# Performance work log

Measured on AMD Instinct MI355X. Metric: run time of the kernel, lower is better.

## Reference

```python
import jax, jax.numpy as jnp
import numpy as np

DIM = 1024

def setup_inputs() -> dict:
    key = jax.random.key(0)
    ks = jax.random.split(key, 7)
    s = 1.0 / np.sqrt(DIM)  # roughly match nn.Linear init scale
    return {
        "x": jax.random.normal(ks[0], (4, 2048, DIM), dtype=jnp.float32),
        "Wq": jax.random.normal(ks[1], (DIM, DIM), dtype=jnp.float32) * s,
        "bq": jax.random.normal(ks[2], (DIM,), dtype=jnp.float32) * s,
        "Wk": jax.random.normal(ks[3], (DIM, DIM), dtype=jnp.float32) * s,
        "bk": jax.random.normal(ks[4], (DIM,), dtype=jnp.float32) * s,
        "Wv": jax.random.normal(ks[5], (DIM, DIM), dtype=jnp.float32) * s,
        "bv": jax.random.normal(ks[6], (DIM,), dtype=jnp.float32) * s,
    }

def reference(x, Wq, bq, Wk, bk, Wv, bv):
    # torch Linear: y = x @ W.T + b
    C = x.shape[-1]
    scale = C ** (-0.5)
    q = jnp.einsum('bnc,dc->bnd', x, Wq) + bq
    k = jnp.einsum('bnc,dc->bnd', x, Wk) + bk
    v = jnp.einsum('bnc,dc->bnd', x, Wv) + bv
    attn = jnp.einsum('bnd,bmd->bnm', q, k) * scale  # [B,N,N]
    attn = jax.nn.softmax(attn, axis=-1)
    out = jnp.einsum('bnm,bmd->bnd', attn, v)
    return out
```

## Files before the change

### kernel.cpp

```cpp
#include <hip/hip_runtime.h>

#define SEQ  2048
#define DIM  1024
#define NTOK 8192
#define NQKV 3072

typedef __attribute__((ext_vector_type(8))) __bf16 bf16x8;
typedef __attribute__((ext_vector_type(4))) float  f32x4;

__device__ __forceinline__ unsigned short f2bf(float f) {
    unsigned int u = __float_as_uint(f);
    u += 0x7fffu + ((u >> 16) & 1u);
    return (unsigned short)(u >> 16);
}

__device__ __forceinline__ float bfu2f(unsigned int lo16) {
    return __uint_as_float(lo16 << 16);
}

__device__ __forceinline__ void load_lds_128(const unsigned short* g, unsigned short* l) {
    __builtin_amdgcn_global_load_lds(
        (const __attribute__((address_space(1))) void*)g,
        (__attribute__((address_space(3))) void*)l, 16, 0, 0);
}

#define BAR() asm volatile("s_barrier" ::: "memory")

template <int MODE>
__global__ __launch_bounds__(512, 2)
void gemm256(const unsigned short* __restrict__ A, const unsigned short* __restrict__ B,
             void* __restrict__ Cv,
             const float* __restrict__ b0v, const float* __restrict__ b1v,
             const float* __restrict__ b2v, unsigned short* __restrict__ vt,
             float* __restrict__ rsv,
             int K, int lda, int ldb, int ldc,
             long sA, long sB, long sC, float alpha)
{
    constexpr int AT = 256 * 64;
    constexpr int BT = 128 * 64;
    __shared__ __align__(16) unsigned short As[3 * AT];
    __shared__ __align__(16) unsigned short Bs[3 * BT];

    const int tid  = threadIdx.x;
    const int wave = tid >> 6;
    const int lane = tid & 63;
    const int l4   = lane & 15;
    const int lh   = lane >> 4;
    const int wm   = wave >> 1;
    const int wn   = wave & 1;

    const int m0 = blockIdx.x * 256;
    const int n0 = blockIdx.y * 128;
    const int z  = blockIdx.z;
    A += (long)z * sA;
    B += (long)z * sB;

    const int r0 = tid >> 3;
    const int gc = (tid & 7) ^ (r0 & 7);
    const unsigned short* Ag = A + (long)(m0 + r0) * lda + gc * 8;
    const unsigned short* Bg = B + (long)(n0 + r0) * ldb + gc * 8;
    unsigned short* Al = As + tid * 8;
    unsigned short* Bl = Bs + tid * 8;

    const int NT = K >> 6;

    auto stage = [&](int t, int slot, int ph) {
        const long kof = (long)t * 64;
        unsigned short* al = Al + slot * AT;
        unsigned short* bl = Bl + slot * BT;
        if (ph == 0) {
            load_lds_128(Ag + kof,                          al);
            load_lds_128(Ag + kof + (long)64 * lda,         al + 4096);
            load_lds_128(Bg + kof,                          bl);
        } else {
            load_lds_128(Ag + kof + (long)128 * lda,        al + 8192);
            load_lds_128(Ag + kof + (long)192 * lda,        al + 12288);
            load_lds_128(Bg + kof + (long)64 * ldb,         bl + 4096);
        }
    };

    const int aoff = (wm * 64 + l4) * 64;
    const int boff = (wn * 64 + l4) * 64;
    const int cs0  = ((0 + lh) ^ (lane & 7)) * 8;
    const int cs1  = ((4 + lh) ^ (lane & 7)) * 8;

    f32x4 acc[4][4] = {};
    bf16x8 a0[4], b0[4], a1[4], b1[4];

    auto ldfrag = [&](bf16x8 (&a)[4], bf16x8 (&b)[4],
                      const unsigned short* Ab, const unsigned short* Bb, int cs) {
#pragma unroll
        for (int mf = 0; mf < 4; ++mf) a[mf] = *(const bf16x8*)(Ab + mf * 1024 + cs);
#pragma unroll
        for (int nf = 0; nf < 4; ++nf) b[nf] = *(const bf16x8*)(Bb + nf * 1024 + cs);
    };
    auto mfma16 = [&](bf16x8 (&a)[4], bf16x8 (&b)[4]) {
        __builtin_amdgcn_s_setprio(1);
#pragma unroll
        for (int mf = 0; mf < 4; ++mf)
#pragma unroll
            for (int nf = 0; nf < 4; ++nf)
                acc[mf][nf] = __builtin_amdgcn_mfma_f32_16x16x32_bf16(
                    a[mf], b[nf], acc[mf][nf], 0, 0, 0);
        __builtin_amdgcn_s_setprio(0);
    };

    stage(0, 0, 0); stage(0, 0, 1);
    stage(1, 1, 0); stage(1, 1, 1);
    asm volatile("s_waitcnt vmcnt(6)" ::: "memory");
    BAR();
    ldfrag(a0, b0, As + aoff, Bs + boff, cs0);

    int sl = 0;
    for (int t = 0; t < NT; ++t) {
        const unsigned short* Ab = As + sl * AT + aoff;
        const unsigned short* Bb = Bs + sl * BT + boff;
        const int st  = (sl >= 1) ? sl - 1 : 2;
        const int nsl = (sl == 2) ? 0 : sl + 1;

        ldfrag(a1, b1, Ab, Bb, cs1);
        if (t + 2 < NT) stage(t + 2, st, 0);
        mfma16(a0, b0);

        if (t + 2 < NT) stage(t + 2, st, 1);
        asm volatile("s_waitcnt lgkmcnt(0)" ::: "memory");
        if (t < NT - 2) asm volatile("s_waitcnt vmcnt(6)" ::: "memory");
        else            asm volatile("s_waitcnt vmcnt(0)" ::: "memory");
        BAR();
        if (t + 1 < NT)
            ldfrag(a0, b0, As + nsl * AT + aoff, Bs + nsl * BT + boff, cs0);
        mfma16(a1, b1);
        sl = nsl;
    }

    const int r0c = m0 + wm * 64 + lh * 4;
    const int c0c = n0 + wn * 64 + l4;

    if (MODE == 0) {
        if (n0 >= 2048) {
#pragma unroll
            for (int nf = 0; nf < 4; ++nf) {
                const int d = c0c + nf * 16 - 2048;
                const float bias = b2v[d];
#pragma unroll
                for (int mf = 0; mf < 4; ++mf) {
                    const int row = r0c + mf * 16;
                    const int bb = row >> 11;
                    const int mm = row & 2047;
                    ushort4 u;
                    u.x = f2bf(acc[mf][nf][0] + bias);
                    u.y = f2bf(acc[mf][nf][1] + bias);
                    u.z = f2bf(acc[mf][nf][2] + bias);
                    u.w = f2bf(acc[mf][nf][3] + bias);
                    *(ushort4*)(vt + ((long)bb * DIM + d) * SEQ + mm) = u;
                }
            }
        } else {
            unsigned short* C16 = (unsigned short*)Cv;
#pragma unroll
            for (int nf = 0; nf < 4; ++nf) {
                const int col = c0c + nf * 16;
                const float bias = (col >= 1024) ? b1v[col - 1024] : b0v[col];
#pragma unroll
                for (int mf = 0; mf < 4; ++mf)
#pragma unroll
                    for (int r = 0; r < 4; ++r)
                        C16[(long)(r0c + mf * 16 + r) * ldc + col] =
                            f2bf(acc[mf][nf][r] + bias);
            }
        }
    } else if (MODE == 1) {
        float* C = (float*)Cv + (long)z * sC;
        const float* rsp = rsv + (long)z * SEQ;
#pragma unroll
        for (int mf = 0; mf < 4; ++mf) {
            const int rowb = r0c + mf * 16;
            const float4 rs4 = *(const float4*)(rsp + rowb);
            const float i0 = 1.0f / rs4.x, i1 = 1.0f / rs4.y;
            const float i2 = 1.0f / rs4.z, i3 = 1.0f / rs4.w;
#pragma unroll
            for (int nf = 0; nf < 4; ++nf) {
                const int col = c0c + nf * 16;
                C[(long)(rowb + 0) * ldc + col] = acc[mf][nf][0] * i0;
                C[(long)(rowb + 1) * ldc + col] = acc[mf][nf][1] * i1;
                C[(long)(rowb + 2) * ldc + col] = acc[mf][nf][2] * i2;
                C[(long)(rowb + 3) * ldc + col] = acc[mf][nf][3] * i3;
            }
        }
    } else {
        unsigned short* C16 = (unsigned short*)Cv + (long)z * sC;
        float* rs = rsv + (long)z * SEQ;
#pragma unroll
        for (int mf = 0; mf < 4; ++mf)
#pragma unroll
            for (int r = 0; r < 4; ++r) {
                const int rowi = r0c + mf * 16 + r;
                float s = 0.f;
#pragma unroll
                for (int nf = 0; nf < 4; ++nf) {
                    const int col = c0c + nf * 16;
                    const unsigned short pu = f2bf(__expf(acc[mf][nf][r] * alpha));
                    C16[(long)rowi * ldc + col] = pu;
                    s += bfu2f(pu);
                }
                s += __shfl_xor(s, 1);
                s += __shfl_xor(s, 2);
                s += __shfl_xor(s, 4);
                s += __shfl_xor(s, 8);
                if (l4 == 0) atomicAdd(rs + rowi, s);
            }
    }
}

#define PREP_BLOCKS (8192 + 3072 + 32)

__global__ __launch_bounds__(256)
void prep(const float* __restrict__ x,
          const float* __restrict__ Wq, const float* __restrict__ Wk,
          const float* __restrict__ Wv,
          unsigned short* __restrict__ xb, unsigned short* __restrict__ Wb,
          float* __restrict__ rs)
{
    const int b = blockIdx.x;
    if (b < 8192) {
        const int i = b * 256 + threadIdx.x;
        float4 f = ((const float4*)x)[i];
        ushort4 u;
        u.x = f2bf(f.x); u.y = f2bf(f.y); u.z = f2bf(f.z); u.w = f2bf(f.w);
        ((ushort4*)xb)[i] = u;
    } else if (b < 8192 + 3072) {
        const int idx = (b - 8192) * 256 + threadIdx.x;
        const int sel = idx / (DIM * DIM / 4);
        const int j   = idx - sel * (DIM * DIM / 4);
        const float* src = (sel == 0) ? Wq : ((sel == 1) ? Wk : Wv);
        float4 f = ((const float4*)src)[j];
        ushort4 u;
        u.x = f2bf(f.x); u.y = f2bf(f.y); u.z = f2bf(f.z); u.w = f2bf(f.w);
        ((ushort4*)(Wb + (long)sel * DIM * DIM))[j] = u;
    } else {
        const int idx = (b - 8192 - 3072) * 256 + threadIdx.x;
        if (idx < NTOK) rs[idx] = 0.f;
    }
}

extern "C" void kernel_launch(void* const* d_in, const int* in_sizes, int n_in,
                              void* d_out, int out_size, void* d_ws, size_t ws_size,
                              hipStream_t stream)
{
    const float* x  = (const float*)d_in[0];
    const float* Wq = (const float*)d_in[1];
    const float* bq = (const float*)d_in[2];
    const float* Wk = (const float*)d_in[3];
    const float* bk = (const float*)d_in[4];
    const float* Wv = (const float*)d_in[5];
    const float* bv = (const float*)d_in[6];
    float* out = (float*)d_out;

    char* ws = (char*)d_ws;
    unsigned short* xb   = (unsigned short*)ws;
    unsigned short* Wb   = (unsigned short*)(ws + 16u * 1024 * 1024);
    unsigned short* qkv  = (unsigned short*)(ws + 64u * 1024 * 1024);
    unsigned short* vt   = (unsigned short*)(ws + 112u * 1024 * 1024);
    unsigned short* P    = (unsigned short*)(ws + 128u * 1024 * 1024);
    float*          rs   = (float*)(ws + 160u * 1024 * 1024);

    const float scale = 0.03125f;
    dim3 blk512(512);

    prep<<<PREP_BLOCKS, 256, 0, stream>>>(x, Wq, Wk, Wv, xb, Wb, rs);

    gemm256<0><<<dim3(NTOK / 256, NQKV / 128), blk512, 0, stream>>>(
        xb, Wb, qkv, bq, bk, bv, vt, nullptr,
        DIM, DIM, DIM, NQKV, 0, 0, 0, 1.0f);

    gemm256<2><<<dim3(SEQ / 256, SEQ / 128, 4), blk512, 0, stream>>>(
        qkv, qkv + 1024, P, nullptr, nullptr, nullptr, nullptr, rs,
        DIM, NQKV, NQKV, SEQ,
        (long)SEQ * NQKV, (long)SEQ * NQKV, (long)SEQ * SEQ, scale);

    gemm256<1><<<dim3(SEQ / 256, DIM / 128, 4), blk512, 0, stream>>>(
        P, vt, out, nullptr, nullptr, nullptr, nullptr, rs,
        SEQ, SEQ, SEQ, DIM,
        (long)SEQ * SEQ, (long)DIM * SEQ, (long)SEQ * DIM, 1.0f);
}
```

Before: 243.6 us.

## Add dedicated triple-buffered PV GEMM kernel with fragment double-buffering

Replaces the generic gemm256<1> for the P·V product with a specialized kernel. It uses a three-slot LDS ring for asynchronous global-to-LDS loads, split into two phases per tile, and double-buffered register fragments so MFMA work overlaps both the LDS reads and the global loads. MFMA sections run at raised wave priority via s_setprio. The cost is more LDS per block (about 144KB for three stages), which may limit occupancy, and hand-tuned waitcnt logic that must match the number of outstanding loads.

```diff
diff --git a/kernel.cpp b/kernel.cpp
--- a/kernel.cpp
+++ b/kernel.cpp
@@ -169,24 +169,6 @@
                             f2bf(acc[mf][nf][r] + bias);
             }
         }
-    } else if (MODE == 1) {
-        float* C = (float*)Cv + (long)z * sC;
-        const float* rsp = rsv + (long)z * SEQ;
-#pragma unroll
-        for (int mf = 0; mf < 4; ++mf) {
-            const int rowb = r0c + mf * 16;
-            const float4 rs4 = *(const float4*)(rsp + rowb);
-            const float i0 = 1.0f / rs4.x, i1 = 1.0f / rs4.y;
-            const float i2 = 1.0f / rs4.z, i3 = 1.0f / rs4.w;
-#pragma unroll
-            for (int nf = 0; nf < 4; ++nf) {
-                const int col = c0c + nf * 16;
-                C[(long)(rowb + 0) * ldc + col] = acc[mf][nf][0] * i0;
-                C[(long)(rowb + 1) * ldc + col] = acc[mf][nf][1] * i1;
-                C[(long)(rowb + 2) * ldc + col] = acc[mf][nf][2] * i2;
-                C[(long)(rowb + 3) * ldc + col] = acc[mf][nf][3] * i3;
-            }
-        }
     } else {
         unsigned short* C16 = (unsigned short*)Cv + (long)z * sC;
         float* rs = rsv + (long)z * SEQ;
@@ -209,6 +191,130 @@
                 s += __shfl_xor(s, 8);
                 if (l4 == 0) atomicAdd(rs + rowi, s);
             }
+    }
+}
+
+__global__ __launch_bounds__(512, 2)
+void gemm_pv(const unsigned short* __restrict__ A, const unsigned short* __restrict__ B,
+             float* __restrict__ C, const float* __restrict__ rsv,
+             int K, int lda, int ldb, int ldc,
+             long sA, long sB, long sC)
+{
+    constexpr int AT = 256 * 64;
+    constexpr int BT = 128 * 64;
+    __shared__ __align__(16) unsigned short As[3 * AT];
+    __shared__ __align__(16) unsigned short Bs[3 * BT];
+
+    const int tid  = threadIdx.x;
+    const int wave = tid >> 6;
+    const int lane = tid & 63;
+    const int l4   = lane & 15;
+    const int lh   = lane >> 4;
+    const int wm   = wave >> 1;
+    const int wn   = wave & 1;
+
+    const int m0 = blockIdx.x * 256;
+    const int n0 = blockIdx.y * 128;
+    const int z  = blockIdx.z;
+    A += (long)z * sA;
+    B += (long)z * sB;
+
+    const int r0 = tid >> 3;
+    const int gc = (tid & 7) ^ (r0 & 7);
+    const unsigned short* Ag = A + (long)(m0 + r0) * lda + gc * 8;
+    const unsigned short* Bg = B + (long)(n0 + r0) * ldb + gc * 8;
+    unsigned short* Al = As + tid * 8;
+    unsigned short* Bl = Bs + tid * 8;
+
+    const int NT = K >> 6;
+
+    auto stage = [&](int t, int slot, int ph) {
+        const long kof = (long)t * 64;
+        unsigned short* al = Al + slot * AT;
+        unsigned short* bl = Bl + slot * BT;
+        if (ph == 0) {
+            load_lds_128(Ag + kof,                          al);
+            load_lds_128(Ag + kof + (long)64 * lda,         al + 4096);
+            load_lds_128(Bg + kof,                          bl);
+        } else {
+            load_lds_128(Ag + kof + (long)128 * lda,        al + 8192);
+            load_lds_128(Ag + kof + (long)192 * lda,        al + 12288);
+            load_lds_128(Bg + kof + (long)64 * ldb,         bl + 4096);
+        }
+    };
+
+    const int aoff = (wm * 64 + l4) * 64;
+    const int boff = (wn * 64 + l4) * 64;
+    const int cs0  = ((0 + lh) ^ (lane & 7)) * 8;
+    const int cs1  = ((4 + lh) ^ (lane & 7)) * 8;
+
+    f32x4 acc[4][4] = {};
+    bf16x8 a0[4], b0[4], a1[4], b1[4];
+
+    auto ldfrag = [&](bf16x8 (&a)[4], bf16x8 (&b)[4],
+                      const unsigned short* Ab, const unsigned short* Bb, int cs) {
+#pragma unroll
+        for (int mf = 0; mf < 4; ++mf) a[mf] = *(const bf16x8*)(Ab + mf * 1024 + cs);
+#pragma unroll
+        for (int nf = 0; nf < 4; ++nf) b[nf] = *(const bf16x8*)(Bb + nf * 1024 + cs);
+    };
+    auto mfma16 = [&](bf16x8 (&a)[4], bf16x8 (&b)[4]) {
+        __builtin_amdgcn_s_setprio(1);
+#pragma unroll
+        for (int mf = 0; mf < 4; ++mf)
+#pragma unroll
+            for (int nf = 0; nf < 4; ++nf)
+                acc[mf][nf] = __builtin_amdgcn_mfma_f32_16x16x32_bf16(
+                    a[mf], b[nf], acc[mf][nf], 0, 0, 0);
+        __builtin_amdgcn_s_setprio(0);
+    };
+
+    stage(0, 0, 0); stage(0, 0, 1);
+    stage(1, 1, 0); stage(1, 1, 1);
+    asm volatile("s_waitcnt vmcnt(6)" ::: "memory");
+    BAR();
+    ldfrag(a0, b0, As + aoff, Bs + boff, cs0);
+
+    int sl = 0;
+    for (int t = 0; t < NT; ++t) {
+        const unsigned short* Ab = As + sl * AT + aoff;
+        const unsigned short* Bb = Bs + sl * BT + boff;
+        const int st  = (sl >= 1) ? sl - 1 : 2;
+        const int nsl = (sl == 2) ? 0 : sl + 1;
+
+        ldfrag(a1, b1, Ab, Bb, cs1);
+        if (t + 2 < NT) stage(t + 2, st, 0);
+        mfma16(a0, b0);
+
+        if (t + 2 < NT) stage(t + 2, st, 1);
+        asm volatile("s_waitcnt lgkmcnt(0)" ::: "memory");
+        if (t < NT - 2) asm volatile("s_waitcnt vmcnt(6)" ::: "memory");
+        else            asm volatile("s_waitcnt vmcnt(0)" ::: "memory");
+        BAR();
+        if (t + 1 < NT)
+            ldfrag(a0, b0, As + nsl * AT + aoff, Bs + nsl * BT + boff, cs0);
+        mfma16(a1, b1);
+        sl = nsl;
+    }
+
+    float* Cz = C + (long)z * sC;
+    const float* rsp = rsv + (long)z * SEQ;
+    const int r0c = m0 + wm * 64 + lh * 4;
+    const int c0c = n0 + wn * 64 + l4;
+#pragma unroll
+    for (int mf = 0; mf < 4; ++mf) {
+        const int rowb = r0c + mf * 16;
+        const float4 rs4 = *(const float4*)(rsp + rowb);
+        const float i0 = 1.0f / rs4.x, i1 = 1.0f / rs4.y;
+        const float i2 = 1.0f / rs4.z, i3 = 1.0f / rs4.w;
+#pragma unroll
+        for (int nf = 0; nf < 4; ++nf) {
+            const int col = c0c + nf * 16;
+            Cz[(long)(rowb + 0) * ldc + col] = acc[mf][nf][0] * i0;
+            Cz[(long)(rowb + 1) * ldc + col] = acc[mf][nf][1] * i1;
+            Cz[(long)(rowb + 2) * ldc + col] = acc[mf][nf][2] * i2;
+            Cz[(long)(rowb + 3) * ldc + col] = acc[mf][nf][3] * i3;
+        }
     }
 }
 
@@ -278,8 +384,8 @@
         DIM, NQKV, NQKV, SEQ,
         (long)SEQ * NQKV, (long)SEQ * NQKV, (long)SEQ * SEQ, scale);
 
-    gemm256<1><<<dim3(SEQ / 256, DIM / 128, 4), blk512, 0, stream>>>(
-        P, vt, out, nullptr, nullptr, nullptr, nullptr, rs,
+    gemm_pv<<<dim3(SEQ / 256, DIM / 128, 4), blk512, 0, stream>>>(
+        P, vt, out, rs,
         SEQ, SEQ, SEQ, DIM,
-        (long)SEQ * SEQ, (long)DIM * SEQ, (long)SEQ * DIM, 1.0f);
-}
+        (long)SEQ * SEQ, (long)DIM * SEQ, (long)SEQ * DIM);
+}
```

After: 243.8 us. About the same (+0.1%).
